# Kernel tuning notes

Hardware: AMD Instinct MI355X
Metric: run time of the kernel (lower is better)

The kernel has to match this reference:

```python
import jax, jax.numpy as jnp
import numpy as np

B, D, H, O, E, K = 16384, 128, 512, 128, 8, 2
T = 1.0
EPS = float(np.finfo(float).eps)  # combine() zero-fill epsilon


def cv_squared(v):
    # torch .var() is unbiased (ddof=1)
    return jnp.var(v, ddof=1) / (jnp.mean(v) ** 2 + 1e-10)


def setup_inputs() -> dict:
    key = jax.random.key(0)
    k0, k1, k2, k3, k4, k5 = jax.random.split(key, 6)
    x = jax.random.normal(k0, (B, D), dtype=jnp.float32)
    w_gate = jax.random.normal(k1, (D, E), dtype=jnp.float32) * 0.02
    w1 = jax.random.normal(k2, (E, D, H), dtype=jnp.float32) * (1.0 / np.sqrt(D))
    b1 = jax.random.normal(k3, (E, H), dtype=jnp.float32) * 0.01
    w2 = jax.random.normal(k4, (E, H, O), dtype=jnp.float32) * (1.0 / np.sqrt(H))
    b2 = jax.random.normal(k5, (E, O), dtype=jnp.float32) * 0.01
    return {"x": x, "w_gate": w_gate, "w1": w1, "b1": b1, "w2": w2, "b2": b2}


def reference(x, w_gate, w1, b1, w2, b2):
    # ---- noisy top-k gating (eval mode: clean logits, no noise) ----
    logits = x @ w_gate                                   # [B, E]
    top_logits, top_idx = jax.lax.top_k(logits, K)        # [B, K]
    top_gates = jax.nn.softmax(top_logits / T, axis=-1)   # [B, K]
    gates = jnp.zeros_like(logits).at[jnp.arange(x.shape[0])[:, None], top_idx].set(top_gates)

    importance = gates.sum(0)                              # [E]
    load = (gates > 0).sum(0).astype(jnp.float32)          # [E]
    loss = cv_squared(importance) + cv_squared(load)

    # ---- experts (dense gate-weighted form of dispatch/combine) ----
    # output[b] = Sum_i gates[b,i] * expert_i(x[b]); zero gates contribute nothing,
    # identical math to SparseDispatcher's gather / per-expert MLP / scatter-add.
    h = jax.nn.relu(jnp.einsum('bd,edh->beh', x, w1) + b1[None])   # [B, E, H]
    y_e = jnp.einsum('beh,eho->beo', h, w2) + b2[None]             # [B, E, O]
    y = jnp.einsum('be,beo->bo', gates, y_e)                       # [B, O]
    # combine(): combined[combined == 0] = eps
    y = jnp.where(y == 0, jnp.asarray(EPS, y.dtype), y)
    return y, loss
```

## Files before the change

kernel.cpp:

```cpp
#include <hip/hip_runtime.h>
#include <hip/hip_bf16.h>
#include <math.h>

#define NB 16384
#define ND 128
#define NH 512
#define NO 128
#define NE 8
#define CPAD 32
#define NCH 8
#define EPSF 2.2204460492503131e-16f

using bf16x8 = __attribute__((ext_vector_type(8))) short;
using f32x16 = __attribute__((ext_vector_type(16))) float;
using uint2v = __attribute__((ext_vector_type(2))) unsigned;

#define WS_COUNTS 0u
#define WS_IMP    1024u
#define WS_TOKID  2048u
#define WS_TOKGG  526336u
#define WS_XBF    657408u
#define WS_W1F    4851712u
#define WS_W2F    5900288u
#define WS_YSTAGE 6948864u

__device__ __forceinline__ unsigned f2bf(float f){
  unsigned u = __float_as_uint(f);
  u += 0x7FFFu + ((u >> 16) & 1u);
  return u >> 16;
}
__device__ __forceinline__ unsigned cvtpk(float lo, float hi){
  unsigned r;
  asm("v_cvt_pk_bf16_f32 %0, %1, %2" : "=v"(r) : "v"(lo), "v"(hi));
  return r;
}
__device__ __forceinline__ void gld16(const void* g, void* l){
  __builtin_amdgcn_global_load_lds((const __attribute__((address_space(1))) void*)g,
                                   (__attribute__((address_space(3))) void*)l, 16, 0, 0);
}

__global__ __launch_bounds__(256) void prep_kernel(
    const float* __restrict__ x, const float* __restrict__ wg,
    const float* __restrict__ w1, const float* __restrict__ w2,
    unsigned short* __restrict__ xbf, unsigned short* __restrict__ w1f,
    unsigned short* __restrict__ w2f, int* __restrict__ counts,
    float* __restrict__ imp, int* __restrict__ tok_ids, float2* __restrict__ tok_gg){
  int bx = blockIdx.x, tid = threadIdx.x;
  if (bx >= 512){
    int u = (bx - 512)*256 + tid;
    int o = u & 127, hb = (u>>7)&7, c = (u>>10)&7, e = u>>13;
    int h0 = c*64 + (hb>>1)*16 + (hb&1)*8;
    const float* src = w2 + (size_t)e*NH*NO + (size_t)h0*NO + o;
    unsigned q[4];
    #pragma unroll
    for (int p = 0; p < 4; ++p)
      q[p] = f2bf(src[(2*p)*NO]) | (f2bf(src[(2*p+1)*NO]) << 16);
    *(uint4*)(w2f + (size_t)u*8) = make_uint4(q[0], q[1], q[2], q[3]);
    return;
  }
  if (bx >= 256){
    int u = (bx - 256)*256 + tid;
    int h32 = u & 31, db = (u>>5)&15, hf = (u>>9)&1, c = (u>>10)&7, e = u>>13;
    int d0 = (db>>1)*16 + (db&1)*8;
    int hg = c*64 + hf*32 + h32;
    const float* src = w1 + (size_t)e*ND*NH + (size_t)d0*NH + hg;
    unsigned q[4];
    #pragma unroll
    for (int p = 0; p < 4; ++p)
      q[p] = f2bf(src[(2*p)*NH]) | (f2bf(src[(2*p+1)*NH]) << 16);
    *(uint4*)(w1f + (size_t)u*8) = make_uint4(q[0], q[1], q[2], q[3]);
    return;
  }
  __shared__ int   lcnt[NE];
  __shared__ float limp[NE];
  __shared__ int   lbase[NE];
  if (tid < NE){ lcnt[tid] = 0; limp[tid] = 0.f; }
  __syncthreads();
  int tok  = bx*64 + (tid >> 2);
  int part = tid & 3;
  const float4* xr4 = (const float4*)(x + (size_t)tok*ND);
  double acc[NE];
  #pragma unroll
  for (int e = 0; e < NE; ++e) acc[e] = 0.0;
  #pragma unroll
  for (int j = 0; j < 8; ++j){
    int f4 = part + j*4;
    float4 v = xr4[f4];
    uint2 p;
    p.x = f2bf(v.x) | (f2bf(v.y) << 16);
    p.y = f2bf(v.z) | (f2bf(v.w) << 16);
    *(uint2*)(xbf + (size_t)tok*ND + f4*4) = p;
    const float4* wr = (const float4*)(wg + f4*32);
    float vm[4] = {v.x, v.y, v.z, v.w};
    #pragma unroll
    for (int m = 0; m < 4; ++m){
      float4 wa = wr[2*m], wb = wr[2*m+1];
      double d = (double)vm[m];
      acc[0] += d*(double)wa.x; acc[1] += d*(double)wa.y;
      acc[2] += d*(double)wa.z; acc[3] += d*(double)wa.w;
      acc[4] += d*(double)wb.x; acc[5] += d*(double)wb.y;
      acc[6] += d*(double)wb.z; acc[7] += d*(double)wb.w;
    }
  }
  #pragma unroll
  for (int e = 0; e < NE; ++e){
    acc[e] += __shfl_xor(acc[e], 1);
    acc[e] += __shfl_xor(acc[e], 2);
  }
  int i0 = 0, i1 = 0, s0 = 0, s1 = 0;
  float g0 = 0.f, g1 = 0.f;
  if (part == 0){
    double l0 = acc[0];
    #pragma unroll
    for (int e = 1; e < NE; ++e) if (acc[e] > l0){ l0 = acc[e]; i0 = e; }
    i1 = (i0 == 0) ? 1 : 0;
    double l1 = acc[i1];
    #pragma unroll
    for (int e = 0; e < NE; ++e) if (e != i0 && acc[e] > l1){ l1 = acc[e]; i1 = e; }
    float e1 = expf((float)(l1 - l0));
    g0 = 1.0f/(1.0f + e1);
    g1 = e1/(1.0f + e1);
    s0 = atomicAdd(&lcnt[i0], 1);
    s1 = atomicAdd(&lcnt[i1], 1);
    atomicAdd(&limp[i0], g0);
    atomicAdd(&limp[i1], g1);
    tok_gg[tok] = make_float2(g0, g1);
  }
  __syncthreads();
  if (tid < NE){
    lbase[tid] = atomicAdd(&counts[tid*CPAD], lcnt[tid]);
    atomicAdd(&imp[tid*CPAD], limp[tid]);
  }
  __syncthreads();
  if (part == 0){
    tok_ids[i0*NB + lbase[i0] + s0] = tok;
    tok_ids[i1*NB + lbase[i1] + s1] = tok | (1 << 30);
  }
}

__global__ __launch_bounds__(256) void expert_kernel(
    const unsigned short* __restrict__ xbf, const unsigned short* __restrict__ w1f,
    const unsigned short* __restrict__ w2f, const float* __restrict__ b1,
    const float* __restrict__ b2, const int* __restrict__ counts,
    const int* __restrict__ tok_ids, float* __restrict__ ystage){
  __shared__ char smem[65536];
  int e = blockIdx.y;
  int n_e = counts[e*CPAD];
  int base = blockIdx.x*128;
  if (base >= n_e) return;
  int tid = threadIdx.x, wid = tid >> 6, lane = tid & 63, l31 = lane & 31, hi = lane >> 5;
  const int* tid_e = tok_ids + e*NB;
  char* w1buf = smem;
  char* w2buf = smem + 32768;
  const char* g1base = (const char*)w1f + ((size_t)e*NCH)*16384;
  const char* g2base = (const char*)w2f + ((size_t)e*NCH)*16384;

  int slot0 = base + wid*32 + l31;
  int raw0 = tid_e[slot0 < n_e ? slot0 : n_e-1];
  int tok0 = raw0 & 0x3FFFFFFF;
  bf16x8 xfrag[8];
  #pragma unroll
  for (int k = 0; k < 8; ++k)
    xfrag[k] = *(const bf16x8*)(xbf + (size_t)tok0*ND + (k*2 + hi)*8);

#define STAGE(c, bsel) do { \
    const char* _g1 = g1base + (size_t)(c)*16384 + wid*1024 + lane*16; \
    const char* _g2 = g2base + (size_t)(c)*16384 + wid*1024 + lane*16; \
    char* _l1 = w1buf + (bsel)*16384 + wid*1024; \
    char* _l2 = w2buf + (bsel)*16384 + wid*1024; \
    _Pragma("unroll") \
    for (int _s = 0; _s < 4; ++_s){ \
      gld16(_g1 + _s*4096, _l1 + _s*4096); \
      gld16(_g2 + _s*4096, _l2 + _s*4096); \
    } \
  } while(0)

  STAGE(0, 0);
  f32x16 yacc[4];
  #pragma unroll
  for (int ot = 0; ot < 4; ++ot)
    #pragma unroll
    for (int i = 0; i < 16; ++i) yacc[ot][i] = 0.f;
  __syncthreads();

  for (int c = 0; c < NCH; ++c){
    int b = c & 1;
    if (c + 1 < NCH) STAGE(c + 1, b ^ 1);
    bf16x8 aht[4];
    #pragma unroll
    for (int hf = 0; hf < 2; ++hf){
      f32x16 hacc;
      #pragma unroll
      for (int i = 0; i < 16; ++i) hacc[i] = 0.f;
      #pragma unroll
      for (int k = 0; k < 8; ++k){
        bf16x8 a = *(const bf16x8*)(w1buf + b*16384 + hf*8192 + (k*2 + hi)*512 + l31*16);
        hacc = __builtin_amdgcn_mfma_f32_32x32x16_bf16(a, xfrag[k], hacc, 0, 0, 0);
      }
      const float4* b1p = (const float4*)(b1 + e*NH + c*64 + hf*32 + hi*4);
      float dv[16];
      #pragma unroll
      for (int g = 0; g < 4; ++g){
        float4 bv = b1p[2*g];
        dv[4*g+0] = fmaxf(hacc[4*g+0] + bv.x, 0.f);
        dv[4*g+1] = fmaxf(hacc[4*g+1] + bv.y, 0.f);
        dv[4*g+2] = fmaxf(hacc[4*g+2] + bv.z, 0.f);
        dv[4*g+3] = fmaxf(hacc[4*g+3] + bv.w, 0.f);
      }
      unsigned A0 = cvtpk(dv[0], dv[1]),  A1 = cvtpk(dv[2], dv[3]);
      unsigned A2 = cvtpk(dv[4], dv[5]),  A3 = cvtpk(dv[6], dv[7]);
      unsigned A4 = cvtpk(dv[8], dv[9]),  A5 = cvtpk(dv[10], dv[11]);
      unsigned A6 = cvtpk(dv[12], dv[13]), A7 = cvtpk(dv[14], dv[15]);
      uint2v r0 = __builtin_amdgcn_permlane32_swap(A0, A2, false, false);
      uint2v r1 = __builtin_amdgcn_permlane32_swap(A1, A3, false, false);
      uint2v r2 = __builtin_amdgcn_permlane32_swap(A4, A6, false, false);
      uint2v r3 = __builtin_amdgcn_permlane32_swap(A5, A7, false, false);
      union { unsigned u[4]; bf16x8 v; } fa, fb;
      fa.u[0] = r0[0]; fa.u[1] = r1[0]; fa.u[2] = r0[1]; fa.u[3] = r1[1];
      fb.u[0] = r2[0]; fb.u[1] = r3[0]; fb.u[2] = r2[1]; fb.u[3] = r3[1];
      aht[hf*2 + 0] = fa.v;
      aht[hf*2 + 1] = fb.v;
    }
    #pragma unroll
    for (int ot = 0; ot < 4; ++ot)
      #pragma unroll
      for (int kk = 0; kk < 4; ++kk){
        bf16x8 bfr = *(const bf16x8*)(w2buf + b*16384 + (kk*2 + hi)*2048 + (ot*32 + l31)*16);
        yacc[ot] = __builtin_amdgcn_mfma_f32_32x32x16_bf16(aht[kk], bfr, yacc[ot], 0, 0, 0);
      }
    __syncthreads();
  }
#undef STAGE
  float b2v[4];
  #pragma unroll
  for (int ot = 0; ot < 4; ++ot) b2v[ot] = b2[e*NO + ot*32 + l31];
  #pragma unroll
  for (int r = 0; r < 16; ++r){
    int row = (r & 3) + 8*(r >> 2) + 4*hi;
    int slot = base + wid*32 + row;
    if (slot < n_e){
      int rw = tid_e[slot];
      int tk = rw & 0x3FFFFFFF, wh = (rw >> 30) & 1;
      float* dst = ystage + ((size_t)tk*2 + wh)*NO + l31;
      #pragma unroll
      for (int ot = 0; ot < 4; ++ot)
        dst[ot*32] = yacc[ot][r] + b2v[ot];
    }
  }
}

__global__ __launch_bounds__(256) void combine_kernel(
    const float* __restrict__ ystage, const float2* __restrict__ tok_gg,
    const int* __restrict__ counts, const float* __restrict__ imp,
    float* __restrict__ y){
  if (blockIdx.x == 0 && threadIdx.x == 0){
    double si = 0, sqi = 0, sl = 0, sql = 0;
    for (int e = 0; e < NE; ++e){
      double a = imp[e*CPAD];
      double b = (double)counts[e*CPAD];
      si += a; sqi += a*a; sl += b; sql += b*b;
    }
    double mi = si/8.0, vi = (sqi - 8.0*mi*mi)/7.0;
    double ml = sl/8.0, vl = (sql - 8.0*ml*ml)/7.0;
    y[NB*NO] = (float)(vi/(mi*mi + 1e-10) + vl/(ml*ml + 1e-10));
  }
  int idx = blockIdx.x*256 + threadIdx.x;
  int tk = idx >> 5, q = idx & 31;
  float2 gg = tok_gg[tk];
  float4 a = *(const float4*)(ystage + (size_t)tk*256 + q*4);
  float4 b = *(const float4*)(ystage + (size_t)tk*256 + 128 + q*4);
  float4 v;
  v.x = gg.x*a.x + gg.y*b.x;  v.x = (v.x == 0.f) ? EPSF : v.x;
  v.y = gg.x*a.y + gg.y*b.y;  v.y = (v.y == 0.f) ? EPSF : v.y;
  v.z = gg.x*a.z + gg.y*b.z;  v.z = (v.z == 0.f) ? EPSF : v.z;
  v.w = gg.x*a.w + gg.y*b.w;  v.w = (v.w == 0.f) ? EPSF : v.w;
  *(float4*)(y + (size_t)tk*128 + q*4) = v;
}

extern "C" void kernel_launch(void* const* d_in, const int* in_sizes, int n_in,
                              void* d_out, int out_size, void* d_ws, size_t ws_size,
                              hipStream_t stream){
  (void)in_sizes; (void)n_in; (void)out_size; (void)ws_size;
  const float* x  = (const float*)d_in[0];
  const float* wg = (const float*)d_in[1];
  const float* w1 = (const float*)d_in[2];
  const float* b1 = (const float*)d_in[3];
  const float* w2 = (const float*)d_in[4];
  const float* b2 = (const float*)d_in[5];
  float* out = (float*)d_out;
  char* ws = (char*)d_ws;
  int*            counts  = (int*)(ws + WS_COUNTS);
  float*          imp     = (float*)(ws + WS_IMP);
  int*            tok_ids = (int*)(ws + WS_TOKID);
  float2*         tok_gg  = (float2*)(ws + WS_TOKGG);
  unsigned short* xbf     = (unsigned short*)(ws + WS_XBF);
  unsigned short* w1f     = (unsigned short*)(ws + WS_W1F);
  unsigned short* w2f     = (unsigned short*)(ws + WS_W2F);
  float*          ystage  = (float*)(ws + WS_YSTAGE);

  hipMemsetAsync(d_ws, 0, 2048, stream);
  prep_kernel<<<768, 256, 0, stream>>>(x, wg, w1, w2, xbf, w1f, w2f,
                                       counts, imp, tok_ids, tok_gg);
  expert_kernel<<<dim3(128, NE), 256, 0, stream>>>(xbf, w1f, w2f, b1, b2,
                                                   counts, tok_ids, ystage);
  combine_kernel<<<2048, 256, 0, stream>>>(ystage, tok_gg, counts, imp, out);
}
```

Before: 56.64 us.

## Compact expert grid, halve LDS chunks, store gated bf16 staging output

The expert kernel now launches a compact 1D grid of 264 blocks. Each block finds its expert and token range from a prefix over the per-expert counts, so the up to 1024 blocks of the old 2D grid, most of which exited early, are gone. The H chunk shrinks from 64 to 32, which halves shared memory to 32 KB to allow higher occupancy, and the weight prep layout changes to match. The gate multiply moves into the expert epilogue and the staging buffer is stored as bf16, which halves staging traffic and simplifies the combine kernel. The cost is extra bf16 rounding on outputs and more loop iterations with more barriers.

```diff
diff --git a/kernel.cpp b/kernel.cpp
--- a/kernel.cpp
+++ b/kernel.cpp
@@ -8,7 +8,7 @@
 #define NO 128
 #define NE 8
 #define CPAD 32
-#define NCH 8
+#define NCH 16
 #define EPSF 2.2204460492503131e-16f
 
 using bf16x8 = __attribute__((ext_vector_type(8))) short;
@@ -48,8 +48,8 @@
   int bx = blockIdx.x, tid = threadIdx.x;
   if (bx >= 512){
     int u = (bx - 512)*256 + tid;
-    int o = u & 127, hb = (u>>7)&7, c = (u>>10)&7, e = u>>13;
-    int h0 = c*64 + (hb>>1)*16 + (hb&1)*8;
+    int o = u & 127, hb = (u>>7)&3, c = (u>>9)&15, e = u>>13;
+    int h0 = c*32 + (hb>>1)*16 + (hb&1)*8;
     const float* src = w2 + (size_t)e*NH*NO + (size_t)h0*NO + o;
     unsigned q[4];
     #pragma unroll
@@ -60,9 +60,9 @@
   }
   if (bx >= 256){
     int u = (bx - 256)*256 + tid;
-    int h32 = u & 31, db = (u>>5)&15, hf = (u>>9)&1, c = (u>>10)&7, e = u>>13;
+    int h32 = u & 31, db = (u>>5)&15, c = (u>>9)&15, e = u>>13;
     int d0 = (db>>1)*16 + (db&1)*8;
-    int hg = c*64 + hf*32 + h32;
+    int hg = c*32 + h32;
     const float* src = w1 + (size_t)e*ND*NH + (size_t)d0*NH + hg;
     unsigned q[4];
     #pragma unroll
@@ -142,18 +142,28 @@
     const unsigned short* __restrict__ xbf, const unsigned short* __restrict__ w1f,
     const unsigned short* __restrict__ w2f, const float* __restrict__ b1,
     const float* __restrict__ b2, const int* __restrict__ counts,
-    const int* __restrict__ tok_ids, float* __restrict__ ystage){
-  __shared__ char smem[65536];
-  int e = blockIdx.y;
-  int n_e = counts[e*CPAD];
-  int base = blockIdx.x*128;
-  if (base >= n_e) return;
+    const int* __restrict__ tok_ids, const float2* __restrict__ tok_gg,
+    unsigned short* __restrict__ ystage){
+  __shared__ char smem[32768];
+  int b = blockIdx.x;
+  int e = 0, base = 0, accb = 0, n_e = 0;
+  #pragma unroll
+  for (int ee = 0; ee < NE; ++ee){
+    int ne = counts[ee*CPAD];
+    int nbl = (ne + 127) >> 7;
+    if (e == 0 && base == 0 && b < accb + nbl && n_e == 0){
+      e = ee; base = (b - accb)*128; n_e = ne;
+    }
+    accb += nbl;
+  }
+  if (b >= accb) return;
+  if (n_e == 0) return;
   int tid = threadIdx.x, wid = tid >> 6, lane = tid & 63, l31 = lane & 31, hi = lane >> 5;
   const int* tid_e = tok_ids + e*NB;
   char* w1buf = smem;
-  char* w2buf = smem + 32768;
-  const char* g1base = (const char*)w1f + ((size_t)e*NCH)*16384;
-  const char* g2base = (const char*)w2f + ((size_t)e*NCH)*16384;
+  char* w2buf = smem + 16384;
+  const char* g1base = (const char*)w1f + ((size_t)e*NCH)*8192;
+  const char* g2base = (const char*)w2f + ((size_t)e*NCH)*8192;
 
   int slot0 = base + wid*32 + l31;
   int raw0 = tid_e[slot0 < n_e ? slot0 : n_e-1];
@@ -164,12 +174,12 @@
     xfrag[k] = *(const bf16x8*)(xbf + (size_t)tok0*ND + (k*2 + hi)*8);
 
 #define STAGE(c, bsel) do { \
-    const char* _g1 = g1base + (size_t)(c)*16384 + wid*1024 + lane*16; \
-    const char* _g2 = g2base + (size_t)(c)*16384 + wid*1024 + lane*16; \
-    char* _l1 = w1buf + (bsel)*16384 + wid*1024; \
-    char* _l2 = w2buf + (bsel)*16384 + wid*1024; \
+    const char* _g1 = g1base + (size_t)(c)*8192 + wid*1024 + lane*16; \
+    const char* _g2 = g2base + (size_t)(c)*8192 + wid*1024 + lane*16; \
+    char* _l1 = w1buf + (bsel)*8192 + wid*1024; \
+    char* _l2 = w2buf + (bsel)*8192 + wid*1024; \
     _Pragma("unroll") \
-    for (int _s = 0; _s < 4; ++_s){ \
+    for (int _s = 0; _s < 2; ++_s){ \
       gld16(_g1 + _s*4096, _l1 + _s*4096); \
       gld16(_g2 + _s*4096, _l2 + _s*4096); \
     } \
@@ -184,50 +194,45 @@
   __syncthreads();
 
   for (int c = 0; c < NCH; ++c){
-    int b = c & 1;
-    if (c + 1 < NCH) STAGE(c + 1, b ^ 1);
-    bf16x8 aht[4];
-    #pragma unroll
-    for (int hf = 0; hf < 2; ++hf){
-      f32x16 hacc;
-      #pragma unroll
-      for (int i = 0; i < 16; ++i) hacc[i] = 0.f;
-      #pragma unroll
-      for (int k = 0; k < 8; ++k){
-        bf16x8 a = *(const bf16x8*)(w1buf + b*16384 + hf*8192 + (k*2 + hi)*512 + l31*16);
-        hacc = __builtin_amdgcn_mfma_f32_32x32x16_bf16(a, xfrag[k], hacc, 0, 0, 0);
-      }
-      const float4* b1p = (const float4*)(b1 + e*NH + c*64 + hf*32 + hi*4);
-      float dv[16];
-      #pragma unroll
-      for (int g = 0; g < 4; ++g){
-        float4 bv = b1p[2*g];
-        dv[4*g+0] = fmaxf(hacc[4*g+0] + bv.x, 0.f);
-        dv[4*g+1] = fmaxf(hacc[4*g+1] + bv.y, 0.f);
-        dv[4*g+2] = fmaxf(hacc[4*g+2] + bv.z, 0.f);
-        dv[4*g+3] = fmaxf(hacc[4*g+3] + bv.w, 0.f);
-      }
-      unsigned A0 = cvtpk(dv[0], dv[1]),  A1 = cvtpk(dv[2], dv[3]);
-      unsigned A2 = cvtpk(dv[4], dv[5]),  A3 = cvtpk(dv[6], dv[7]);
-      unsigned A4 = cvtpk(dv[8], dv[9]),  A5 = cvtpk(dv[10], dv[11]);
-      unsigned A6 = cvtpk(dv[12], dv[13]), A7 = cvtpk(dv[14], dv[15]);
-      uint2v r0 = __builtin_amdgcn_permlane32_swap(A0, A2, false, false);
-      uint2v r1 = __builtin_amdgcn_permlane32_swap(A1, A3, false, false);
-      uint2v r2 = __builtin_amdgcn_permlane32_swap(A4, A6, false, false);
-      uint2v r3 = __builtin_amdgcn_permlane32_swap(A5, A7, false, false);
-      union { unsigned u[4]; bf16x8 v; } fa, fb;
-      fa.u[0] = r0[0]; fa.u[1] = r1[0]; fa.u[2] = r0[1]; fa.u[3] = r1[1];
-      fb.u[0] = r2[0]; fb.u[1] = r3[0]; fb.u[2] = r2[1]; fb.u[3] = r3[1];
-      aht[hf*2 + 0] = fa.v;
-      aht[hf*2 + 1] = fb.v;
-    }
-    #pragma unroll
-    for (int ot = 0; ot < 4; ++ot)
-      #pragma unroll
-      for (int kk = 0; kk < 4; ++kk){
-        bf16x8 bfr = *(const bf16x8*)(w2buf + b*16384 + (kk*2 + hi)*2048 + (ot*32 + l31)*16);
-        yacc[ot] = __builtin_amdgcn_mfma_f32_32x32x16_bf16(aht[kk], bfr, yacc[ot], 0, 0, 0);
-      }
+    int bb = c & 1;
+    if (c + 1 < NCH) STAGE(c + 1, bb ^ 1);
+    f32x16 hacc;
+    #pragma unroll
+    for (int i = 0; i < 16; ++i) hacc[i] = 0.f;
+    #pragma unroll
+    for (int k = 0; k < 8; ++k){
+      bf16x8 a = *(const bf16x8*)(w1buf + bb*8192 + (k*2 + hi)*512 + l31*16);
+      hacc = __builtin_amdgcn_mfma_f32_32x32x16_bf16(a, xfrag[k], hacc, 0, 0, 0);
+    }
+    const float4* b1p = (const float4*)(b1 + e*NH + c*32 + hi*4);
+    float dv[16];
+    #pragma unroll
+    for (int g = 0; g < 4; ++g){
+      float4 bv = b1p[2*g];
+      dv[4*g+0] = fmaxf(hacc[4*g+0] + bv.x, 0.f);
+      dv[4*g+1] = fmaxf(hacc[4*g+1] + bv.y, 0.f);
+      dv[4*g+2] = fmaxf(hacc[4*g+2] + bv.z, 0.f);
+      dv[4*g+3] = fmaxf(hacc[4*g+3] + bv.w, 0.f);
+    }
+    unsigned A0 = cvtpk(dv[0], dv[1]),  A1 = cvtpk(dv[2], dv[3]);
+    unsigned A2 = cvtpk(dv[4], dv[5]),  A3 = cvtpk(dv[6], dv[7]);
+    unsigned A4 = cvtpk(dv[8], dv[9]),  A5 = cvtpk(dv[10], dv[11]);
+    unsigned A6 = cvtpk(dv[12], dv[13]), A7 = cvtpk(dv[14], dv[15]);
+    uint2v r0 = __builtin_amdgcn_permlane32_swap(A0, A2, false, false);
+    uint2v r1 = __builtin_amdgcn_permlane32_swap(A1, A3, false, false);
+    uint2v r2 = __builtin_amdgcn_permlane32_swap(A4, A6, false, false);
+    uint2v r3 = __builtin_amdgcn_permlane32_swap(A5, A7, false, false);
+    union { unsigned u[4]; bf16x8 v; } fa, fb;
+    fa.u[0] = r0[0]; fa.u[1] = r1[0]; fa.u[2] = r0[1]; fa.u[3] = r1[1];
+    fb.u[0] = r2[0]; fb.u[1] = r3[0]; fb.u[2] = r2[1]; fb.u[3] = r3[1];
+    bf16x8 aht0 = fa.v, aht1 = fb.v;
+    #pragma unroll
+    for (int ot = 0; ot < 4; ++ot){
+      bf16x8 bf0 = *(const bf16x8*)(w2buf + bb*8192 + (0*2 + hi)*2048 + (ot*32 + l31)*16);
+      yacc[ot] = __builtin_amdgcn_mfma_f32_32x32x16_bf16(aht0, bf0, yacc[ot], 0, 0, 0);
+      bf16x8 bf1 = *(const bf16x8*)(w2buf + bb*8192 + (1*2 + hi)*2048 + (ot*32 + l31)*16);
+      yacc[ot] = __builtin_amdgcn_mfma_f32_32x32x16_bf16(aht1, bf1, yacc[ot], 0, 0, 0);
+    }
     __syncthreads();
   }
 #undef STAGE
@@ -241,18 +246,19 @@
     if (slot < n_e){
       int rw = tid_e[slot];
       int tk = rw & 0x3FFFFFFF, wh = (rw >> 30) & 1;
-      float* dst = ystage + ((size_t)tk*2 + wh)*NO + l31;
+      float2 gg = tok_gg[tk];
+      float g = wh ? gg.y : gg.x;
+      unsigned short* dst = ystage + ((size_t)tk*2 + wh)*NO + l31;
       #pragma unroll
       for (int ot = 0; ot < 4; ++ot)
-        dst[ot*32] = yacc[ot][r] + b2v[ot];
+        dst[ot*32] = (unsigned short)f2bf((yacc[ot][r] + b2v[ot]) * g);
     }
   }
 }
 
 __global__ __launch_bounds__(256) void combine_kernel(
-    const float* __restrict__ ystage, const float2* __restrict__ tok_gg,
-    const int* __restrict__ counts, const float* __restrict__ imp,
-    float* __restrict__ y){
+    const unsigned short* __restrict__ ystage, const int* __restrict__ counts,
+    const float* __restrict__ imp, float* __restrict__ y){
   if (blockIdx.x == 0 && threadIdx.x == 0){
     double si = 0, sqi = 0, sl = 0, sql = 0;
     for (int e = 0; e < NE; ++e){
@@ -265,16 +271,24 @@
     y[NB*NO] = (float)(vi/(mi*mi + 1e-10) + vl/(ml*ml + 1e-10));
   }
   int idx = blockIdx.x*256 + threadIdx.x;
-  int tk = idx >> 5, q = idx & 31;
-  float2 gg = tok_gg[tk];
-  float4 a = *(const float4*)(ystage + (size_t)tk*256 + q*4);
-  float4 b = *(const float4*)(ystage + (size_t)tk*256 + 128 + q*4);
-  float4 v;
-  v.x = gg.x*a.x + gg.y*b.x;  v.x = (v.x == 0.f) ? EPSF : v.x;
-  v.y = gg.x*a.y + gg.y*b.y;  v.y = (v.y == 0.f) ? EPSF : v.y;
-  v.z = gg.x*a.z + gg.y*b.z;  v.z = (v.z == 0.f) ? EPSF : v.z;
-  v.w = gg.x*a.w + gg.y*b.w;  v.w = (v.w == 0.f) ? EPSF : v.w;
-  *(float4*)(y + (size_t)tk*128 + q*4) = v;
+  int tk = idx >> 4, q = idx & 15;
+  const unsigned short* r0 = ystage + (size_t)tk*256 + q*8;
+  uint4 a = *(const uint4*)r0;
+  uint4 bq = *(const uint4*)(r0 + 128);
+  unsigned aw[4] = {a.x, a.y, a.z, a.w};
+  unsigned bw[4] = {bq.x, bq.y, bq.z, bq.w};
+  float4 o0, o1;
+  float* op[8] = {&o0.x,&o0.y,&o0.z,&o0.w,&o1.x,&o1.y,&o1.z,&o1.w};
+  #pragma unroll
+  for (int i = 0; i < 4; ++i){
+    float vlo = __uint_as_float(aw[i] << 16)        + __uint_as_float(bw[i] << 16);
+    float vhi = __uint_as_float(aw[i] & 0xFFFF0000u) + __uint_as_float(bw[i] & 0xFFFF0000u);
+    *op[2*i]   = (vlo == 0.f) ? EPSF : vlo;
+    *op[2*i+1] = (vhi == 0.f) ? EPSF : vhi;
+  }
+  float* dst = y + (size_t)tk*128 + q*8;
+  *(float4*)dst     = o0;
+  *(float4*)(dst+4) = o1;
 }
 
 extern "C" void kernel_launch(void* const* d_in, const int* in_sizes, int n_in,
@@ -296,12 +310,12 @@
   unsigned short* xbf     = (unsigned short*)(ws + WS_XBF);
   unsigned short* w1f     = (unsigned short*)(ws + WS_W1F);
   unsigned short* w2f     = (unsigned short*)(ws + WS_W2F);
-  float*          ystage  = (float*)(ws + WS_YSTAGE);
+  unsigned short* ystage  = (unsigned short*)(ws + WS_YSTAGE);
 
   hipMemsetAsync(d_ws, 0, 2048, stream);
   prep_kernel<<<768, 256, 0, stream>>>(x, wg, w1, w2, xbf, w1f, w2f,
                                        counts, imp, tok_ids, tok_gg);
-  expert_kernel<<<dim3(128, NE), 256, 0, stream>>>(xbf, w1f, w2f, b1, b2,
-                                                   counts, tok_ids, ystage);
-  combine_kernel<<<2048, 256, 0, stream>>>(ystage, tok_gg, counts, imp, out);
-}
+  expert_kernel<<<264, 256, 0, stream>>>(xbf, w1f, w2f, b1, b2,
+                                         counts, tok_ids, tok_gg, ystage);
+  combine_kernel<<<1024, 256, 0, stream>>>(ystage, counts, imp, out);
+}
```

Measured after the change: 55.12 us. 2.7% less time.
